# Kernel optimization log

Measured on AMD Instinct MI355X. Metric: run time of the kernel, lower is better.

The kernel has to match this reference:

```python
import jax, jax.numpy as jnp
import numpy as np

B, T, I, H = 256, 2048, 64, 256


def setup_inputs() -> dict:
    key = jax.random.key(0)
    ks = jax.random.split(key, 8)
    s_ih = 1.0 / np.sqrt(H)
    return {
        "x": jax.random.normal(ks[0], (B, T, I), dtype=jnp.float32),
        "lengths": jax.random.randint(ks[1], (B,), 1, T + 1),  # in [1, T]
        "W_ih": jax.random.uniform(ks[2], (H, I), minval=-s_ih, maxval=s_ih),
        "W_hh": jax.random.uniform(ks[3], (H, H), minval=-s_ih, maxval=s_ih),
        "b_ih": jax.random.uniform(ks[4], (H,), minval=-s_ih, maxval=s_ih),
        "b_hh": jax.random.uniform(ks[5], (H,), minval=-s_ih, maxval=s_ih),
        "W_fc": jax.random.uniform(ks[6], (1, H), minval=-s_ih, maxval=s_ih),
        "b_fc": jax.random.uniform(ks[7], (1,), minval=-s_ih, maxval=s_ih),
    }


def reference(x, lengths, W_ih, W_hh, b_ih, b_hh, W_fc, b_fc):
    # Vanilla RNN (tanh), batch_first: h_t = tanh(x_t W_ih^T + b_ih + h_{t-1} W_hh^T + b_hh)
    batch = x.shape[0]
    h0 = jnp.zeros((batch, W_hh.shape[0]), dtype=x.dtype)
    # Precompute input projections for all timesteps in one big GEMM: [B, T, H]
    xp = jnp.einsum("bti,hi->bth", x, W_ih) + b_ih + b_hh

    def step(h, xt):  # xt: [B, H]
        h = jnp.tanh(xt + h @ W_hh.T)
        return h, h

    _, hs = jax.lax.scan(step, h0, jnp.swapaxes(xp, 0, 1))  # hs: [T, B, H]
    out = jnp.swapaxes(hs, 0, 1)  # [B, T, H]
    # Per-sample last valid timestep gather
    last = out[jnp.arange(batch), lengths - 1]  # [B, H]
    return last @ W_fc.T + b_fc  # [B, 1]
```

## Files before the change

### kernel.cpp

```cpp
#include <hip/hip_runtime.h>


static constexpr int nB = 256;
static constexpr int nT = 2048;
static constexpr int nI = 64;
static constexpr int nH = 256;
static constexpr int XPB = 16;
static constexpr int XPS = nH + 4;
static constexpr int THREADS = 512;

typedef _Float16 f16x8 __attribute__((ext_vector_type(8)));
typedef float f32x4 __attribute__((ext_vector_type(4)));

__device__ __forceinline__ void barrier_lgkm() {
  asm volatile("s_waitcnt lgkmcnt(0)\n\ts_barrier" ::: "memory");
}

__device__ __forceinline__ float fast_tanh(float x) {
  float a = fabsf(x);
  float e = __expf(-2.0f * a);
  float r = (1.0f - e) / (1.0f + e);
  return copysignf(r, x);
}

__global__ __launch_bounds__(THREADS, 2)
void rnn_v4(const float* __restrict__ x, const int* __restrict__ lengths,
            const float* __restrict__ Wih, const float* __restrict__ Whh,
            const float* __restrict__ bih, const float* __restrict__ bhh,
            const float* __restrict__ Wfc, const float* __restrict__ bfc,
            float* __restrict__ out)
{
  __shared__ __align__(16) _Float16 hbuf[2][nH];
  __shared__ __align__(16) float xpb[2][XPB * XPS];
  __shared__ float red[8];

  const int b   = blockIdx.x;
  const int tid = threadIdx.x;
  const int w   = tid >> 6;
  const int l   = tid & 63;
  const int q   = l >> 4;
  const int n   = l & 15;
  const int len = lengths[b];
  const float* xb = x + (size_t)b * nT * nI;

  f16x8 Ah[2][8];
#pragma unroll
  for (int mt = 0; mt < 2; ++mt) {
    const int row = 32 * w + 16 * mt + n;
#pragma unroll
    for (int kt = 0; kt < 8; ++kt) {
      const float* src = Whh + row * nH + 32 * kt + 8 * q;
      f16x8 a;
#pragma unroll
      for (int j = 0; j < 8; ++j) a[j] = (_Float16)src[j];
      Ah[mt][kt] = a;
    }
  }
  f16x8 Bp[2][2];
  float biasp[2];
#pragma unroll
  for (int ntl = 0; ntl < 2; ++ntl) {
    const int hcol = 32 * w + 16 * ntl + n;
#pragma unroll
    for (int kt = 0; kt < 2; ++kt) {
      const float* src = Wih + hcol * nI + 32 * kt + 8 * q;
      f16x8 a;
#pragma unroll
      for (int j = 0; j < 8; ++j) a[j] = (_Float16)src[j];
      Bp[ntl][kt] = a;
    }
    biasp[ntl] = bih[hcol] + bhh[hcol];
  }
  const int mt_sel  = (n >> 2) & 1;
  const int reg_sel = n & 3;
  const int row_own = 32 * w + 16 * mt_sel + 4 * q + reg_sel;

  {
    const float* pr = xb + (size_t)n * nI + 8 * q;
    float4 x0 = *(const float4*)(pr);
    float4 x1 = *(const float4*)(pr + 4);
    float4 x2 = *(const float4*)(pr + 32);
    float4 x3 = *(const float4*)(pr + 36);
    f16x8 A0 = { (_Float16)x0.x,(_Float16)x0.y,(_Float16)x0.z,(_Float16)x0.w,
                 (_Float16)x1.x,(_Float16)x1.y,(_Float16)x1.z,(_Float16)x1.w };
    f16x8 A1 = { (_Float16)x2.x,(_Float16)x2.y,(_Float16)x2.z,(_Float16)x2.w,
                 (_Float16)x3.x,(_Float16)x3.y,(_Float16)x3.z,(_Float16)x3.w };
#pragma unroll
    for (int ntl = 0; ntl < 2; ++ntl) {
      f32x4 c = { biasp[ntl], biasp[ntl], biasp[ntl], biasp[ntl] };
      c = __builtin_amdgcn_mfma_f32_16x16x32_f16(A0, Bp[ntl][0], c, 0, 0, 0);
      c = __builtin_amdgcn_mfma_f32_16x16x32_f16(A1, Bp[ntl][1], c, 0, 0, 0);
      const int hc = 32 * w + 16 * ntl + n;
#pragma unroll
      for (int r = 0; r < 4; ++r) xpb[0][(4 * q + r) * XPS + hc] = c[r];
    }
  }
  if (tid < nH) hbuf[0][tid] = (_Float16)0.f;
  __syncthreads();

  int t = 0;
  for (int blk = 0; t < len; ++blk) {
    const int t0n = (blk + 1) * XPB;
    const bool havenext = t0n < len;
    float4 x0, x1, x2, x3;
    if (havenext) {
      const float* pr = xb + (size_t)(t0n + n) * nI + 8 * q;
      x0 = *(const float4*)(pr);
      x1 = *(const float4*)(pr + 4);
      x2 = *(const float4*)(pr + 32);
      x3 = *(const float4*)(pr + 36);
    }

    const int nsteps = min(XPB, len - blk * XPB);
    const float* xpsrc = xpb[blk & 1];

    for (int s = 0; s < nsteps; ++s, ++t) {
      const _Float16* hsrc = hbuf[t & 1];

      f32x4 acc0 = *(const f32x4*)(xpsrc + s * XPS + 32 * w + 4 * q);
      f32x4 acc1 = *(const f32x4*)(xpsrc + s * XPS + 32 * w + 16 + 4 * q);

#pragma unroll
      for (int kt = 0; kt < 8; ++kt) {
        f16x8 Bh = *(const f16x8*)(hsrc + 32 * kt + 8 * q);
        acc0 = __builtin_amdgcn_mfma_f32_16x16x32_f16(Ah[0][kt], Bh, acc0, 0, 0, 0);
        acc1 = __builtin_amdgcn_mfma_f32_16x16x32_f16(Ah[1][kt], Bh, acc1, 0, 0, 0);
      }

      f32x4 a = mt_sel ? acc1 : acc0;
      float lo = (reg_sel & 1) ? a[1] : a[0];
      float hi = (reg_sel & 1) ? a[3] : a[2];
      float v  = (reg_sel & 2) ? hi : lo;
      float hn = fast_tanh(v);

      if (s == nsteps - 1 && havenext) {
        f16x8 A0 = { (_Float16)x0.x,(_Float16)x0.y,(_Float16)x0.z,(_Float16)x0.w,
                     (_Float16)x1.x,(_Float16)x1.y,(_Float16)x1.z,(_Float16)x1.w };
        f16x8 A1 = { (_Float16)x2.x,(_Float16)x2.y,(_Float16)x2.z,(_Float16)x2.w,
                     (_Float16)x3.x,(_Float16)x3.y,(_Float16)x3.z,(_Float16)x3.w };
        float* dst = xpb[(blk + 1) & 1];
#pragma unroll
        for (int ntl = 0; ntl < 2; ++ntl) {
          f32x4 c = { biasp[ntl], biasp[ntl], biasp[ntl], biasp[ntl] };
          c = __builtin_amdgcn_mfma_f32_16x16x32_f16(A0, Bp[ntl][0], c, 0, 0, 0);
          c = __builtin_amdgcn_mfma_f32_16x16x32_f16(A1, Bp[ntl][1], c, 0, 0, 0);
          const int hc = 32 * w + 16 * ntl + n;
#pragma unroll
          for (int r = 0; r < 4; ++r) dst[(4 * q + r) * XPS + hc] = c[r];
        }
      }

      if (n < 8) hbuf[(t + 1) & 1][row_own] = (_Float16)hn;
      barrier_lgkm();
    }
  }

  float v = 0.f;
  if (tid < nH) v = (float)hbuf[len & 1][tid] * Wfc[tid];
#pragma unroll
  for (int off = 32; off; off >>= 1) v += __shfl_down(v, off);
  if (l == 0) red[w] = v;
  __syncthreads();
  if (tid == 0) {
    float acc = bfc[0];
#pragma unroll
    for (int i = 0; i < 8; ++i) acc += red[i];
    out[b] = acc;
  }
}

extern "C" void kernel_launch(void* const* d_in, const int* in_sizes, int n_in,
                              void* d_out, int out_size, void* d_ws, size_t ws_size,
                              hipStream_t stream) {
  const float* x   = (const float*)d_in[0];
  const int* lens  = (const int*)d_in[1];
  const float* Wih = (const float*)d_in[2];
  const float* Whh = (const float*)d_in[3];
  const float* bih = (const float*)d_in[4];
  const float* bhh = (const float*)d_in[5];
  const float* Wfc = (const float*)d_in[6];
  const float* bfc = (const float*)d_in[7];
  float* out = (float*)d_out;

  rnn_v4<<<nB, THREADS, 0, stream>>>(x, lens, Wih, Whh, bih, bhh, Wfc, bfc, out);
}
```

Measured before the change: 1.268 ms.

## Shrink RNN block to two waves, each owning 128 hidden rows

Reduces the per-batch workgroup from 8 waves to 2. Each wave now holds 128 rows of W_hh in registers and issues 64 MFMAs per timestep instead of 16. Each lane computes two tanh outputs and writes them as a packed f16 pair. The goal is cheaper per-step barriers and LDS synchronisation across fewer waves. The cost is a longer serial MFMA chain per wave, very high register pressure (64 f16x8 A-fragments), and less latency hiding on the critical recurrent path.

New measurement: 2.326 ms. +83.5%, slower.

```diff
diff --git a/kernel.cpp b/kernel.cpp
--- a/kernel.cpp
+++ b/kernel.cpp
@@ -7,9 +7,10 @@
 static constexpr int nH = 256;
 static constexpr int XPB = 16;
 static constexpr int XPS = nH + 4;
-static constexpr int THREADS = 512;
+static constexpr int THREADS = 128;
 
 typedef _Float16 f16x8 __attribute__((ext_vector_type(8)));
+typedef _Float16 f16x2 __attribute__((ext_vector_type(2)));
 typedef float f32x4 __attribute__((ext_vector_type(4)));
 
 __device__ __forceinline__ void barrier_lgkm() {
@@ -23,8 +24,8 @@
   return copysignf(r, x);
 }
 
-__global__ __launch_bounds__(THREADS, 2)
-void rnn_v4(const float* __restrict__ x, const int* __restrict__ lengths,
+__global__ __launch_bounds__(THREADS, 1)
+void rnn_v5(const float* __restrict__ x, const int* __restrict__ lengths,
             const float* __restrict__ Wih, const float* __restrict__ Whh,
             const float* __restrict__ bih, const float* __restrict__ bhh,
             const float* __restrict__ Wfc, const float* __restrict__ bfc,
@@ -32,7 +33,7 @@
 {
   __shared__ __align__(16) _Float16 hbuf[2][nH];
   __shared__ __align__(16) float xpb[2][XPB * XPS];
-  __shared__ float red[8];
+  __shared__ float red[2];
 
   const int b   = blockIdx.x;
   const int tid = threadIdx.x;
@@ -43,10 +44,10 @@
   const int len = lengths[b];
   const float* xb = x + (size_t)b * nT * nI;
 
-  f16x8 Ah[2][8];
+  f16x8 Ah[8][8];
 #pragma unroll
-  for (int mt = 0; mt < 2; ++mt) {
-    const int row = 32 * w + 16 * mt + n;
+  for (int mt = 0; mt < 8; ++mt) {
+    const int row = 128 * w + 16 * mt + n;
 #pragma unroll
     for (int kt = 0; kt < 8; ++kt) {
       const float* src = Whh + row * nH + 32 * kt + 8 * q;
@@ -56,24 +57,25 @@
       Ah[mt][kt] = a;
     }
   }
-  f16x8 Bp[2][2];
-  float biasp[2];
+  f16x8 Bp[8][2];
+  float biasp[8];
 #pragma unroll
-  for (int ntl = 0; ntl < 2; ++ntl) {
-    const int hcol = 32 * w + 16 * ntl + n;
+  for (int c = 0; c < 8; ++c) {
+    const int col = 128 * w + 16 * c + n;
 #pragma unroll
     for (int kt = 0; kt < 2; ++kt) {
-      const float* src = Wih + hcol * nI + 32 * kt + 8 * q;
+      const float* src = Wih + col * nI + 32 * kt + 8 * q;
       f16x8 a;
 #pragma unroll
       for (int j = 0; j < 8; ++j) a[j] = (_Float16)src[j];
-      Bp[ntl][kt] = a;
+      Bp[c][kt] = a;
     }
-    biasp[ntl] = bih[hcol] + bhh[hcol];
+    biasp[c] = bih[col] + bhh[col];
   }
-  const int mt_sel  = (n >> 2) & 1;
-  const int reg_sel = n & 3;
-  const int row_own = 32 * w + 16 * mt_sel + 4 * q + reg_sel;
+
+  const int mtl = n & 7;
+  const int r0  = (n >> 3) << 1;
+  const int own = 128 * w + 16 * mtl + 4 * q + r0;
 
   {
     const float* pr = xb + (size_t)n * nI + 8 * q;
@@ -86,16 +88,17 @@
     f16x8 A1 = { (_Float16)x2.x,(_Float16)x2.y,(_Float16)x2.z,(_Float16)x2.w,
                  (_Float16)x3.x,(_Float16)x3.y,(_Float16)x3.z,(_Float16)x3.w };
 #pragma unroll
-    for (int ntl = 0; ntl < 2; ++ntl) {
-      f32x4 c = { biasp[ntl], biasp[ntl], biasp[ntl], biasp[ntl] };
-      c = __builtin_amdgcn_mfma_f32_16x16x32_f16(A0, Bp[ntl][0], c, 0, 0, 0);
-      c = __builtin_amdgcn_mfma_f32_16x16x32_f16(A1, Bp[ntl][1], c, 0, 0, 0);
-      const int hc = 32 * w + 16 * ntl + n;
+    for (int c = 0; c < 8; ++c) {
+      f32x4 cc = { biasp[c], biasp[c], biasp[c], biasp[c] };
+      cc = __builtin_amdgcn_mfma_f32_16x16x32_f16(A0, Bp[c][0], cc, 0, 0, 0);
+      cc = __builtin_amdgcn_mfma_f32_16x16x32_f16(A1, Bp[c][1], cc, 0, 0, 0);
+      const int col = 128 * w + 16 * c + n;
 #pragma unroll
-      for (int r = 0; r < 4; ++r) xpb[0][(4 * q + r) * XPS + hc] = c[r];
+      for (int r = 0; r < 4; ++r) xpb[0][(4 * q + r) * XPS + col] = cc[r];
     }
   }
-  if (tid < nH) hbuf[0][tid] = (_Float16)0.f;
+  hbuf[0][tid]       = (_Float16)0.f;
+  hbuf[0][tid + 128] = (_Float16)0.f;
   __syncthreads();
 
   int t = 0;
@@ -117,21 +120,30 @@
     for (int s = 0; s < nsteps; ++s, ++t) {
       const _Float16* hsrc = hbuf[t & 1];
 
-      f32x4 acc0 = *(const f32x4*)(xpsrc + s * XPS + 32 * w + 4 * q);
-      f32x4 acc1 = *(const f32x4*)(xpsrc + s * XPS + 32 * w + 16 + 4 * q);
+      f32x4 acc[8];
+#pragma unroll
+      for (int mt = 0; mt < 8; ++mt)
+        acc[mt] = *(const f32x4*)(xpsrc + s * XPS + 128 * w + 16 * mt + 4 * q);
 
 #pragma unroll
       for (int kt = 0; kt < 8; ++kt) {
         f16x8 Bh = *(const f16x8*)(hsrc + 32 * kt + 8 * q);
-        acc0 = __builtin_amdgcn_mfma_f32_16x16x32_f16(Ah[0][kt], Bh, acc0, 0, 0, 0);
-        acc1 = __builtin_amdgcn_mfma_f32_16x16x32_f16(Ah[1][kt], Bh, acc1, 0, 0, 0);
+#pragma unroll
+        for (int mt = 0; mt < 8; ++mt)
+          acc[mt] = __builtin_amdgcn_mfma_f32_16x16x32_f16(Ah[mt][kt], Bh, acc[mt], 0, 0, 0);
       }
 
-      f32x4 a = mt_sel ? acc1 : acc0;
-      float lo = (reg_sel & 1) ? a[1] : a[0];
-      float hi = (reg_sel & 1) ? a[3] : a[2];
-      float v  = (reg_sel & 2) ? hi : lo;
-      float hn = fast_tanh(v);
+      f32x4 s0 = (n & 1) ? acc[1] : acc[0];
+      f32x4 s1 = (n & 1) ? acc[3] : acc[2];
+      f32x4 s2 = (n & 1) ? acc[5] : acc[4];
+      f32x4 s3 = (n & 1) ? acc[7] : acc[6];
+      f32x4 t0v = (n & 2) ? s1 : s0;
+      f32x4 t1v = (n & 2) ? s3 : s2;
+      f32x4 u   = (n & 4) ? t1v : t0v;
+      float va = (n & 8) ? u[2] : u[0];
+      float vb = (n & 8) ? u[3] : u[1];
+      float ha = fast_tanh(va);
+      float hb = fast_tanh(vb);
 
       if (s == nsteps - 1 && havenext) {
         f16x8 A0 = { (_Float16)x0.x,(_Float16)x0.y,(_Float16)x0.z,(_Float16)x0.w,
@@ -140,33 +152,28 @@
                      (_Float16)x3.x,(_Float16)x3.y,(_Float16)x3.z,(_Float16)x3.w };
         float* dst = xpb[(blk + 1) & 1];
 #pragma unroll
-        for (int ntl = 0; ntl < 2; ++ntl) {
-          f32x4 c = { biasp[ntl], biasp[ntl], biasp[ntl], biasp[ntl] };
-          c = __builtin_amdgcn_mfma_f32_16x16x32_f16(A0, Bp[ntl][0], c, 0, 0, 0);
-          c = __builtin_amdgcn_mfma_f32_16x16x32_f16(A1, Bp[ntl][1], c, 0, 0, 0);
-          const int hc = 32 * w + 16 * ntl + n;
+        for (int c = 0; c < 8; ++c) {
+          f32x4 cc = { biasp[c], biasp[c], biasp[c], biasp[c] };
+          cc = __builtin_amdgcn_mfma_f32_16x16x32_f16(A0, Bp[c][0], cc, 0, 0, 0);
+          cc = __builtin_amdgcn_mfma_f32_16x16x32_f16(A1, Bp[c][1], cc, 0, 0, 0);
+          const int col = 128 * w + 16 * c + n;
 #pragma unroll
-          for (int r = 0; r < 4; ++r) dst[(4 * q + r) * XPS + hc] = c[r];
+          for (int r = 0; r < 4; ++r) dst[(4 * q + r) * XPS + col] = cc[r];
         }
       }
 
-      if (n < 8) hbuf[(t + 1) & 1][row_own] = (_Float16)hn;
+      *(f16x2*)&hbuf[(t + 1) & 1][own] = f16x2{ (_Float16)ha, (_Float16)hb };
       barrier_lgkm();
     }
   }
 
-  float v = 0.f;
-  if (tid < nH) v = (float)hbuf[len & 1][tid] * Wfc[tid];
+  float v = (float)hbuf[len & 1][tid]       * Wfc[tid]
+          + (float)hbuf[len & 1][tid + 128] * Wfc[tid + 128];
 #pragma unroll
   for (int off = 32; off; off >>= 1) v += __shfl_down(v, off);
   if (l == 0) red[w] = v;
   __syncthreads();
-  if (tid == 0) {
-    float acc = bfc[0];
-#pragma unroll
-    for (int i = 0; i < 8; ++i) acc += red[i];
-    out[b] = acc;
-  }
+  if (tid == 0) out[b] = red[0] + red[1] + bfc[0];
 }
 
 extern "C" void kernel_launch(void* const* d_in, const int* in_sizes, int n_in,
@@ -182,5 +189,5 @@
   const float* bfc = (const float*)d_in[7];
   float* out = (float*)d_out;
 
-  rnn_v4<<<nB, THREADS, 0, stream>>>(x, lens, Wih, Whh, bih, bhh, Wfc, bfc, out);
+  rnn_v5<<<nB, THREADS, 0, stream>>>(x, lens, Wih, Whh, bih, bhh, Wfc, bfc, out);
 }
```
